# Kernel optimization log

Hardware: AMD Instinct MI355X
Metric: run time of the kernel (lower is better)

## Reference

```python
import jax, jax.numpy as jnp
import numpy as np

B, C, H, W = 8, 128, 192, 192
CROP = 39
LEN = CROP // 2            # 19 -> 38x38 crop
CY = CX = 96               # fixed crop center (original draws random.randint(19, 173))
MARGIN = 1.0


def grid_sample_bilinear(img, grid):
    """Bilinear grid_sample, align_corners=True, zeros padding.
    img: (B,C,H,W); grid: (B,H,W,2) with (x,y) in [-1,1]."""
    _, _, Hi, Wi = img.shape
    gx = (grid[..., 0] + 1.0) * 0.5 * (Wi - 1)   # (B,H,W) source x
    gy = (grid[..., 1] + 1.0) * 0.5 * (Hi - 1)   # (B,H,W) source y
    x0 = jnp.floor(gx)
    y0 = jnp.floor(gy)

    def gather(xf, yf):
        valid = (xf >= 0) & (xf <= Wi - 1) & (yf >= 0) & (yf <= Hi - 1)
        xi = jnp.clip(xf, 0, Wi - 1).astype(jnp.int32)
        yi = jnp.clip(yf, 0, Hi - 1).astype(jnp.int32)
        # per-batch gather: (C,H,W) values at integer (y,x) locations
        v = jax.vmap(lambda im, y, x: im[:, y, x])(img, yi, xi)  # (B,C,H,W)
        return v * valid[:, None, :, :].astype(img.dtype)

    wx1 = gx - x0
    wx0 = 1.0 - wx1
    wy1 = gy - y0
    wy0 = 1.0 - wy1
    w = lambda a: a[:, None, :, :]
    return (w(wx0 * wy0) * gather(x0,       y0)
          + w(wx1 * wy0) * gather(x0 + 1.0, y0)
          + w(wx0 * wy1) * gather(x0,       y0 + 1.0)
          + w(wx1 * wy1) * gather(x0 + 1.0, y0 + 1.0))


def hardnet_loss(anchor, positive, margin=MARGIN):
    """loss_HardNet with anchor_swap=False, batch_reduce='min', triplet_margin."""
    d1 = jnp.sum(anchor * anchor, axis=1)                       # (N,)
    d2 = jnp.sum(positive * positive, axis=1)                   # (N,)
    sq = d1[:, None] + d2[None, :] - 2.0 * (anchor @ positive.T)  # (N,N)
    dm = jnp.sqrt(jnp.maximum(sq, 0.0) + 1e-6) + 1e-8
    n = dm.shape[0]
    pos = jnp.diagonal(dm)                                      # positive distances
    dmod = dm + jnp.eye(n, dtype=dm.dtype) * 10.0               # mask diagonal
    dmod = dmod + jnp.where(dmod < 0.008, 10.0, 0.0)            # mask near-duplicates
    min_neg = jnp.min(dmod, axis=1)                             # hardest negative per anchor
    return jnp.mean(jnp.maximum(margin + pos - min_neg, 0.0))


def setup_inputs() -> dict:
    key = jax.random.key(0)
    k1, k2, k3 = jax.random.split(key, 3)
    feat1 = jax.random.normal(k1, (B, C, H, W), dtype=jnp.float32)
    feat2 = jax.random.normal(k2, (B, C, H, W), dtype=jnp.float32)
    # absolute flow: pixel coordinates in [0, W-1] / [0, H-1]
    aflow = jax.random.uniform(k3, (B, 2, H, W), dtype=jnp.float32) * (W - 1)
    return {"feat1": feat1, "feat2": feat2, "aflow": aflow}


def reference(feat1, feat2, aflow):
    # _aflow_to_grid: pixel coords -> [-1,1] grid (align_corners=True convention)
    gx = aflow[:, 0] * (2.0 / (W - 1)) - 1.0
    gy = aflow[:, 1] * (2.0 / (H - 1)) - 1.0
    grid = jnp.stack([gx, gy], axis=-1)                          # (B,H,W,2)
    grid = jnp.where(jnp.isnan(grid), 9e9, grid)                 # invalid -> out of range
    feat2to1 = grid_sample_bilinear(feat2, grid)                 # warp img2 feats to img1
    s = slice(CY - LEN, CY + LEN)                                # fixed 38x38 crop
    f1 = feat1[:, :, s, s]
    f2 = feat2to1[:, :, s, s]
    a = f1.transpose(0, 2, 3, 1).reshape(-1, C)                  # (B*38*38, C)
    p = f2.transpose(0, 2, 3, 1).reshape(-1, C)
    return hardnet_loss(a, p)
```

## Files before the change

### kernel.cpp

```cpp
#include <hip/hip_runtime.h>
#include <stdint.h>

#define Hh 192
#define Ww 192
#define HW 36864
#define CROPW 38
#define CW2 1444
#define CROPOFF 77
#define NPTS 11552
#define NPAD 11776
#define NMT 92
#define NCT 92
#define NG 5
#define JPB 19
#define NBLK (NG*NMT)
#define SLABB 512
#define CROPB 304
#define BIGF 3.0e38f

typedef short bf16x8 __attribute__((ext_vector_type(8)));
typedef float f32x4 __attribute__((ext_vector_type(4)));
typedef uint32_t u32x4 __attribute__((ext_vector_type(4)));
typedef unsigned short ushort;

__device__ __forceinline__ ushort f2bf(float f) {
  uint32_t b = __float_as_uint(f);
  uint32_t r = b + 0x7fffu + ((b >> 16) & 1u);
  return (ushort)(r >> 16);
}
__device__ __forceinline__ float bf2f(ushort u) {
  return __uint_as_float(((uint32_t)u) << 16);
}

__device__ __forceinline__ void g2l16(const void* g, void* l) {
  __builtin_amdgcn_global_load_lds(
      (const __attribute__((address_space(1))) unsigned int*)g,
      (__attribute__((address_space(3))) unsigned int*)l, 16, 0, 0);
}

__global__ __launch_bounds__(1024) void fused_k(
    const float* __restrict__ feat1, const float* __restrict__ feat2,
    const float* __restrict__ aflow,
    ushort* __restrict__ aB, ushort* __restrict__ pB,
    float* __restrict__ d1, float* __restrict__ d2) {
  __shared__ __align__(16) uint32_t plane[HW];
  int bid = blockIdx.x;
  int t = threadIdx.x;

  if (bid < SLABB) {
    int b = bid >> 6, c = (bid & 63) * 2;
    const float* srcA = feat2 + ((size_t)(b*128 + c)) * HW;
    const float* srcB = srcA + HW;
    #pragma unroll
    for (int k = 0; k < 9; ++k) {
      int i = (k*1024 + t) * 4;
      f32x4 va = *(const f32x4*)(srcA + i);
      f32x4 vb = *(const f32x4*)(srcB + i);
      u32x4 pk;
      #pragma unroll
      for (int j = 0; j < 4; ++j)
        pk[j] = (uint32_t)f2bf(va[j]) | ((uint32_t)f2bf(vb[j]) << 16);
      *(u32x4*)&plane[i] = pk;
    }
    __syncthreads();
    int pbase = b*CW2;
    #pragma unroll
    for (int it = 0; it < 2; ++it) {
      int p = it*1024 + t;
      if (p < CW2) {
        int r = p / CROPW, cx = p % CROPW;
        int y = CROPOFF + r, x = CROPOFF + cx;
        float ax = aflow[((b*2 + 0)*Hh + y)*Ww + x];
        float ay = aflow[((b*2 + 1)*Hh + y)*Ww + x];
        float gxn = ax * (2.0f/(Ww-1)) - 1.0f;
        float gyn = ay * (2.0f/(Hh-1)) - 1.0f;
        float gx = (gxn + 1.0f) * 0.5f * (Ww-1);
        float gy = (gyn + 1.0f) * 0.5f * (Hh-1);
        int xi = min((int)floorf(gx), Ww-2);
        int yi = min((int)floorf(gy), Hh-2);
        float wx1 = gx - (float)xi, wx0 = 1.f - wx1;
        float wy1 = gy - (float)yi, wy0 = 1.f - wy1;
        int cell = yi*Ww + xi;
        uint32_t u00 = plane[cell];
        uint32_t u01 = plane[cell + 1];
        uint32_t u10 = plane[cell + Ww];
        uint32_t u11 = plane[cell + Ww + 1];
        float v0 = wy0*(wx0*bf2f((ushort)u00) + wx1*bf2f((ushort)u01))
                 + wy1*(wx0*bf2f((ushort)u10) + wx1*bf2f((ushort)u11));
        float v1 = wy0*(wx0*bf2f((ushort)(u00>>16)) + wx1*bf2f((ushort)(u01>>16)))
                 + wy1*(wx0*bf2f((ushort)(u10>>16)) + wx1*bf2f((ushort)(u11>>16)));
        ushort q0 = f2bf(v0), q1 = f2bf(v1);
        *(uint32_t*)&pB[(size_t)(pbase + p)*128 + c] = (uint32_t)q0 | ((uint32_t)q1 << 16);
        float f0 = bf2f(q0), f1 = bf2f(q1);
        atomicAdd(&d2[pbase + p], f0*f0 + f1*f1);
      }
    }
  } else if (bid < SLABB + CROPB) {
    ushort* lsh = (ushort*)plane;
    int rb2 = bid - SLABB;
    int b = rb2 / CROPW, r = rb2 % CROPW;
    int y = CROPOFF + r;
    {
      int xo = t & 63, cg = t >> 6;
      if (xo < CROPW) {
        const float* src = feat1 + ((size_t)b*128*HW) + (size_t)y*Ww + CROPOFF + xo;
        #pragma unroll
        for (int k = 0; k < 8; ++k) {
          int cc = cg + k*16;
          lsh[xo*136 + cc] = f2bf(src[(size_t)cc*HW]);
        }
      }
    }
    __syncthreads();
    int chunk = t & 7, p = t >> 3;
    if (p < CROPW) {
      int idx = b*CW2 + r*CROPW + p;
      ushort* dst = aB + (size_t)idx*128 + chunk*16;
      *(bf16x8*)dst       = *(const bf16x8*)&lsh[p*136 + chunk*16];
      *(bf16x8*)(dst + 8) = *(const bf16x8*)&lsh[p*136 + chunk*16 + 8];
      float s = 0.f;
      #pragma unroll
      for (int j = 0; j < 16; ++j) {
        float v = bf2f(lsh[p*136 + chunk*16 + j]);
        s += v*v;
      }
      s += __shfl_xor(s, 1); s += __shfl_xor(s, 2); s += __shfl_xor(s, 4);
      if (chunk == 0) d1[idx] = s;
    }
  } else {
    if (t < NPAD - NPTS) {
      int row = NPTS + t;
      u32x4 z = {0,0,0,0};
      #pragma unroll
      for (int c = 0; c < 8; ++c) {
        *(u32x4*)&aB[(size_t)row*128 + c*16] = z;
        *(u32x4*)&aB[(size_t)row*128 + c*16 + 8] = z;
        *(u32x4*)&pB[(size_t)row*128 + c*16] = z;
        *(u32x4*)&pB[(size_t)row*128 + c*16 + 8] = z;
      }
      d1[row] = 0.f;
      d2[row] = 1e30f;
    }
  }
}

__global__ __launch_bounds__(256, 2) void gemmp_k(
    const ushort* __restrict__ aB, const ushort* __restrict__ pB,
    const float* __restrict__ d1, const float* __restrict__ d2,
    float* __restrict__ pos, float* __restrict__ pmin) {
  __shared__ __align__(16) ushort lB[2][128*128];

  int bid = blockIdx.x;
  int xcd = bid & 7, kk = bid >> 3;
  int start = (xcd < 4) ? xcd*58 : 232 + (xcd-4)*57;
  int L = start + kk;
  int g = L / NMT, tM = L % NMT;
  int j0 = g * JPB;
  int jn = (NCT - j0 < JPB) ? (NCT - j0) : JPB;

  int tid = threadIdx.x;
  int rowg = tid >> 4, cb = (tid & 15) << 4;
  int w = tid >> 6, l = tid & 63;
  int wc = w;
  int lcol = l & 15, hq = l >> 4, rb = hq << 2;
  int rsw = (lcol & 7) << 4;

  {
    const char* gB = (const char*)pB + (size_t)j0 * 128 * 256;
    #pragma unroll
    for (int rnd = 0; rnd < 8; ++rnd) {
      int row = rnd*16 + rowg;
      g2l16(gB + row*256 + (cb ^ ((row&7)<<4)), (char*)lB[0] + row*256 + cb);
    }
  }

  bf16x8 aF[32];
  {
    const char* gA = (const char*)aB + ((size_t)(tM*128 + lcol))*256 + hq*16;
    #pragma unroll
    for (int ma = 0; ma < 8; ++ma)
      #pragma unroll
      for (int ks = 0; ks < 4; ++ks)
        aF[ma*4+ks] = *(const bf16x8*)(gA + ma*16*256 + ks*64);
  }
  __syncthreads();

  float mPart[8] = {BIGF,BIGF,BIGF,BIGF,BIGF,BIGF,BIGF,BIGF};

  for (int it = 0; it < jn; ++it) {
    int j = j0 + it;
    if (it + 1 < jn) {
      const char* gB = (const char*)pB + (size_t)(j+1) * 128 * 256;
      char* dst = (char*)lB[(it+1) & 1];
      #pragma unroll
      for (int rnd = 0; rnd < 8; ++rnd) {
        int row = rnd*16 + rowg;
        g2l16(gB + row*256 + (cb ^ ((row&7)<<4)), dst + row*256 + cb);
      }
    }
    f32x4 d2v[2];
    #pragma unroll
    for (int np = 0; np < 2; ++np)
      d2v[np] = *(const f32x4*)&d2[j*128 + wc*32 + np*16 + rb];

    const char* bufB = (const char*)lB[it & 1];
    f32x4 acc[2][8] = {};
    #pragma unroll
    for (int ks = 0; ks < 4; ++ks) {
      int cbase = ks*64 + (hq << 4);
      bf16x8 bF[2];
      #pragma unroll
      for (int np = 0; np < 2; ++np)
        bF[np] = *(const bf16x8*)(bufB + (wc*32 + np*16 + lcol)*256 + (cbase ^ rsw));
      #pragma unroll
      for (int np = 0; np < 2; ++np)
        #pragma unroll
        for (int ma = 0; ma < 8; ++ma)
          acc[np][ma] = __builtin_amdgcn_mfma_f32_16x16x32_bf16(bF[np], aF[ma*4+ks], acc[np][ma], 0, 0, 0);
    }

    if (j != tM) {
      #pragma unroll
      for (int ma = 0; ma < 8; ++ma)
        #pragma unroll
        for (int np = 0; np < 2; ++np)
          #pragma unroll
          for (int reg = 0; reg < 4; ++reg)
            mPart[ma] = fminf(mPart[ma], fmaf(-2.f, acc[np][ma][reg], d2v[np][reg]));
    } else {
      #pragma unroll
      for (int ma = 0; ma < 8; ++ma) {
        int gi = tM*128 + ma*16 + lcol;
        #pragma unroll
        for (int np = 0; np < 2; ++np)
          #pragma unroll
          for (int reg = 0; reg < 4; ++reg) {
            int gj = j*128 + wc*32 + np*16 + rb + reg;
            float t = fmaf(-2.f, acc[np][ma][reg], d2v[np][reg]);
            if (gi == gj)
              pos[gi] = sqrtf(fmaxf(d1[gi] + t, 0.f) + 1e-6f) + 1e-8f;
            else
              mPart[ma] = fminf(mPart[ma], t);
          }
      }
    }
    __syncthreads();
  }

  #pragma unroll
  for (int ma = 0; ma < 8; ++ma) {
    float u = mPart[ma];
    u = fminf(u, __shfl_xor(u, 16));
    u = fminf(u, __shfl_xor(u, 32));
    mPart[ma] = u;
  }
  __syncthreads();
  float* sm = (float*)lB;
  if (hq == 0) {
    #pragma unroll
    for (int ma = 0; ma < 8; ++ma)
      sm[wc*128 + ma*16 + lcol] = mPart[ma];
  }
  __syncthreads();
  if (tid < 128) {
    int row = tM*128 + tid;
    float u = fminf(fminf(sm[tid], sm[128 + tid]),
                    fminf(sm[256 + tid], sm[384 + tid]));
    pmin[g*NPAD + row] = sqrtf(fmaxf(d1[row] + u, 0.f) + 1e-6f) + 1e-8f;
  }
}

__global__ __launch_bounds__(1024) void fin_k(const float* __restrict__ pos,
                                              const float* __restrict__ pmin,
                                              float* __restrict__ out) {
  float s = 0.f;
  for (int i = threadIdx.x*4; i < NPTS; i += 4096) {
    f32x4 p = *(const f32x4*)&pos[i];
    f32x4 mn;
    #pragma unroll
    for (int jj = 0; jj < 4; ++jj) mn[jj] = p[jj] + 10.f;
    #pragma unroll
    for (int gg = 0; gg < NG; ++gg) {
      f32x4 pm = *(const f32x4*)&pmin[gg*NPAD + i];
      #pragma unroll
      for (int jj = 0; jj < 4; ++jj) mn[jj] = fminf(mn[jj], pm[jj]);
    }
    #pragma unroll
    for (int jj = 0; jj < 4; ++jj)
      s += fmaxf(1.0f + p[jj] - mn[jj], 0.f);
  }
  for (int off = 1; off < 64; off <<= 1) s += __shfl_xor(s, off);
  __shared__ float red[16];
  if ((threadIdx.x & 63) == 0) red[threadIdx.x >> 6] = s;
  __syncthreads();
  if (threadIdx.x == 0) {
    float t = 0.f;
    #pragma unroll
    for (int k = 0; k < 16; ++k) t += red[k];
    out[0] = t / (float)NPTS;
  }
}

extern "C" void kernel_launch(void* const* d_in, const int* in_sizes, int n_in,
                              void* d_out, int out_size, void* d_ws, size_t ws_size,
                              hipStream_t stream) {
  const float* feat1 = (const float*)d_in[0];
  const float* feat2 = (const float*)d_in[1];
  const float* aflow = (const float*)d_in[2];

  char* ws = (char*)d_ws;
  ushort* aB = (ushort*)ws;
  ushort* pB = aB + (size_t)NPAD * 128;
  float*  d1 = (float*)(pB + (size_t)NPAD * 128);
  float*  d2 = d1 + NPAD;
  float*  pos = d2 + NPAD;
  float*  pmin = pos + NPAD;

  hipMemsetAsync(d2, 0, NPTS * sizeof(float), stream);
  hipLaunchKernelGGL(fused_k, dim3(SLABB + CROPB + 1), dim3(1024), 0, stream,
                     feat1, feat2, aflow, aB, pB, d1, d2);
  hipLaunchKernelGGL(gemmp_k, dim3(NBLK), dim3(256), 0, stream,
                     aB, pB, d1, d2, pos, pmin);
  hipLaunchKernelGGL(fin_k, dim3(1), dim3(1024), 0, stream,
                     pos, pmin, (float*)d_out);
}
```

Measured before the change: 88.79 us.

## Use 256-row M tiles with 512-thread blocks and atomicMin row-min reduction

The GEMM+min kernel now gives each block 256 anchor rows (two 128-row halves across 8 waves) that share each staged 128-column B tile in LDS. This halves B-tile loads per MFMA and reduces the column split per block to 9 tiles over 11 groups. Per-group partial minima are no longer written to separate buffers. They are merged with an unsigned atomicMin on positive float bits into one array, initialized in the prep kernel, and the final kernel reads a single min array. The larger blocks raise register and LDS pressure and may lower occupancy.

```diff
diff --git a/kernel.cpp b/kernel.cpp
--- a/kernel.cpp
+++ b/kernel.cpp
@@ -9,11 +9,11 @@
 #define CROPOFF 77
 #define NPTS 11552
 #define NPAD 11776
-#define NMT 92
+#define NTT 46
 #define NCT 92
-#define NG 5
-#define JPB 19
-#define NBLK (NG*NMT)
+#define NG 11
+#define JPB 9
+#define NBLK 506
 #define SLABB 512
 #define CROPB 304
 #define BIGF 3.0e38f
@@ -42,7 +42,8 @@
     const float* __restrict__ feat1, const float* __restrict__ feat2,
     const float* __restrict__ aflow,
     ushort* __restrict__ aB, ushort* __restrict__ pB,
-    float* __restrict__ d1, float* __restrict__ d2) {
+    float* __restrict__ d1, float* __restrict__ d2,
+    unsigned* __restrict__ pmin) {
   __shared__ __align__(16) uint32_t plane[HW];
   int bid = blockIdx.x;
   int t = threadIdx.x;
@@ -128,6 +129,11 @@
       if (chunk == 0) d1[idx] = s;
     }
   } else {
+    #pragma unroll
+    for (int it = 0; it < 12; ++it) {
+      int i = it*1024 + t;
+      if (i < NPAD) pmin[i] = 0x7f800000u;
+    }
     if (t < NPAD - NPTS) {
       int row = NPTS + t;
       u32x4 z = {0,0,0,0};
@@ -144,39 +150,39 @@
   }
 }
 
-__global__ __launch_bounds__(256, 2) void gemmp_k(
+__global__ __launch_bounds__(512, 2) void gemmp_k(
     const ushort* __restrict__ aB, const ushort* __restrict__ pB,
     const float* __restrict__ d1, const float* __restrict__ d2,
-    float* __restrict__ pos, float* __restrict__ pmin) {
+    float* __restrict__ pos, unsigned* __restrict__ pmin) {
   __shared__ __align__(16) ushort lB[2][128*128];
 
   int bid = blockIdx.x;
   int xcd = bid & 7, kk = bid >> 3;
-  int start = (xcd < 4) ? xcd*58 : 232 + (xcd-4)*57;
+  int start = (xcd < 2) ? xcd*64 : 128 + (xcd-2)*63;
   int L = start + kk;
-  int g = L / NMT, tM = L % NMT;
+  int g = L / NTT, tM = L % NTT;
   int j0 = g * JPB;
   int jn = (NCT - j0 < JPB) ? (NCT - j0) : JPB;
 
   int tid = threadIdx.x;
   int rowg = tid >> 4, cb = (tid & 15) << 4;
   int w = tid >> 6, l = tid & 63;
-  int wc = w;
+  int mh = w >> 2, wc = w & 3;
   int lcol = l & 15, hq = l >> 4, rb = hq << 2;
   int rsw = (lcol & 7) << 4;
 
   {
     const char* gB = (const char*)pB + (size_t)j0 * 128 * 256;
     #pragma unroll
-    for (int rnd = 0; rnd < 8; ++rnd) {
-      int row = rnd*16 + rowg;
+    for (int rnd = 0; rnd < 4; ++rnd) {
+      int row = rnd*32 + rowg;
       g2l16(gB + row*256 + (cb ^ ((row&7)<<4)), (char*)lB[0] + row*256 + cb);
     }
   }
 
   bf16x8 aF[32];
   {
-    const char* gA = (const char*)aB + ((size_t)(tM*128 + lcol))*256 + hq*16;
+    const char* gA = (const char*)aB + ((size_t)(tM*256 + mh*128 + lcol))*256 + hq*16;
     #pragma unroll
     for (int ma = 0; ma < 8; ++ma)
       #pragma unroll
@@ -193,8 +199,8 @@
       const char* gB = (const char*)pB + (size_t)(j+1) * 128 * 256;
       char* dst = (char*)lB[(it+1) & 1];
       #pragma unroll
-      for (int rnd = 0; rnd < 8; ++rnd) {
-        int row = rnd*16 + rowg;
+      for (int rnd = 0; rnd < 4; ++rnd) {
+        int row = rnd*32 + rowg;
         g2l16(gB + row*256 + (cb ^ ((row&7)<<4)), dst + row*256 + cb);
       }
     }
@@ -219,7 +225,7 @@
           acc[np][ma] = __builtin_amdgcn_mfma_f32_16x16x32_bf16(bF[np], aF[ma*4+ks], acc[np][ma], 0, 0, 0);
     }
 
-    if (j != tM) {
+    if ((j >> 1) != tM) {
       #pragma unroll
       for (int ma = 0; ma < 8; ++ma)
         #pragma unroll
@@ -230,7 +236,7 @@
     } else {
       #pragma unroll
       for (int ma = 0; ma < 8; ++ma) {
-        int gi = tM*128 + ma*16 + lcol;
+        int gi = tM*256 + mh*128 + ma*16 + lcol;
         #pragma unroll
         for (int np = 0; np < 2; ++np)
           #pragma unroll
@@ -259,35 +265,31 @@
   if (hq == 0) {
     #pragma unroll
     for (int ma = 0; ma < 8; ++ma)
-      sm[wc*128 + ma*16 + lcol] = mPart[ma];
+      sm[(mh*4 + wc)*128 + ma*16 + lcol] = mPart[ma];
   }
   __syncthreads();
-  if (tid < 128) {
-    int row = tM*128 + tid;
-    float u = fminf(fminf(sm[tid], sm[128 + tid]),
-                    fminf(sm[256 + tid], sm[384 + tid]));
-    pmin[g*NPAD + row] = sqrtf(fmaxf(d1[row] + u, 0.f) + 1e-6f) + 1e-8f;
+  if (tid < 256) {
+    int mh2 = tid >> 7, rloc = tid & 127;
+    float u = fminf(fminf(sm[(mh2*4+0)*128 + rloc], sm[(mh2*4+1)*128 + rloc]),
+                    fminf(sm[(mh2*4+2)*128 + rloc], sm[(mh2*4+3)*128 + rloc]));
+    int row = tM*256 + tid;
+    float dm = sqrtf(fmaxf(d1[row] + u, 0.f) + 1e-6f) + 1e-8f;
+    atomicMin(&pmin[row], __float_as_uint(dm));
   }
 }
 
 __global__ __launch_bounds__(1024) void fin_k(const float* __restrict__ pos,
-                                              const float* __restrict__ pmin,
+                                              const unsigned* __restrict__ pmin,
                                               float* __restrict__ out) {
   float s = 0.f;
   for (int i = threadIdx.x*4; i < NPTS; i += 4096) {
     f32x4 p = *(const f32x4*)&pos[i];
-    f32x4 mn;
-    #pragma unroll
-    for (int jj = 0; jj < 4; ++jj) mn[jj] = p[jj] + 10.f;
-    #pragma unroll
-    for (int gg = 0; gg < NG; ++gg) {
-      f32x4 pm = *(const f32x4*)&pmin[gg*NPAD + i];
-      #pragma unroll
-      for (int jj = 0; jj < 4; ++jj) mn[jj] = fminf(mn[jj], pm[jj]);
-    }
-    #pragma unroll
-    for (int jj = 0; jj < 4; ++jj)
-      s += fmaxf(1.0f + p[jj] - mn[jj], 0.f);
+    u32x4 pmu = *(const u32x4*)&pmin[i];
+    #pragma unroll
+    for (int jj = 0; jj < 4; ++jj) {
+      float mn = fminf(p[jj] + 10.f, __uint_as_float(pmu[jj]));
+      s += fmaxf(1.0f + p[jj] - mn, 0.f);
+    }
   }
   for (int off = 1; off < 64; off <<= 1) s += __shfl_xor(s, off);
   __shared__ float red[16];
@@ -314,12 +316,12 @@
   float*  d1 = (float*)(pB + (size_t)NPAD * 128);
   float*  d2 = d1 + NPAD;
   float*  pos = d2 + NPAD;
-  float*  pmin = pos + NPAD;
+  unsigned* pmin = (unsigned*)(pos + NPAD);
 
   hipMemsetAsync(d2, 0, NPTS * sizeof(float), stream);
   hipLaunchKernelGGL(fused_k, dim3(SLABB + CROPB + 1), dim3(1024), 0, stream,
-                     feat1, feat2, aflow, aB, pB, d1, d2);
-  hipLaunchKernelGGL(gemmp_k, dim3(NBLK), dim3(256), 0, stream,
+                     feat1, feat2, aflow, aB, pB, d1, d2, pmin);
+  hipLaunchKernelGGL(gemmp_k, dim3(NBLK), dim3(512), 0, stream,
                      aB, pB, d1, d2, pos, pmin);
   hipLaunchKernelGGL(fin_k, dim3(1), dim3(1024), 0, stream,
                      pos, pmin, (float*)d_out);
```

Measured after the change: 104.4 us. +17.6%, slower.
